# Kernel tuning notes

Hardware: AMD Instinct MI355X
Metric: run time of the kernel (lower is better)

Reference implementation:

```python
import jax, jax.numpy as jnp
import numpy as np

N_NODES = 100000
N_EDGES = 1600000
IN_CH = 128
HEADS = 4
HID = 32
OUT_CH = 128
NEG_SLOPE = 0.2


def setup_inputs() -> dict:
    key = jax.random.key(0)
    ks = jax.random.split(key, 7)
    sc = 1.0 / np.sqrt(IN_CH)
    return {
        "x": jax.random.normal(ks[0], (N_NODES, IN_CH), dtype=jnp.float32),
        "edge_index": jax.random.randint(ks[1], (2, N_EDGES), 0, N_NODES, dtype=jnp.int32),
        "W": jax.random.normal(ks[2], (IN_CH, HEADS * HID), dtype=jnp.float32) * sc,
        "att_src": jax.random.normal(ks[3], (HEADS, HID), dtype=jnp.float32) * sc,
        "att_dst": jax.random.normal(ks[4], (HEADS, HID), dtype=jnp.float32) * sc,
        "lin_w": jax.random.normal(ks[5], (HEADS * HID, OUT_CH), dtype=jnp.float32) * (1.0 / np.sqrt(HEADS * HID)),
        "lin_b": jax.random.normal(ks[6], (OUT_CH,), dtype=jnp.float32) * 0.01,
    }


def reference(x, edge_index, W, att_src, att_dst, lin_w, lin_b):
    N = x.shape[0]
    src, dst = edge_index[0], edge_index[1]
    # node-wise linear transform -> [N, H, C]
    h = (x @ W).reshape(N, HEADS, HID)
    # per-node attention logit components [N, H]
    a_src = jnp.einsum("nhc,hc->nh", h, att_src)
    a_dst = jnp.einsum("nhc,hc->nh", h, att_dst)
    # per-edge logits with LeakyReLU [E, H]
    e = jax.nn.leaky_relu(a_src[src] + a_dst[dst], negative_slope=NEG_SLOPE)
    # segment softmax over destination neighborhoods
    m = jax.ops.segment_max(e, dst, num_segments=N)
    ex = jnp.exp(e - m[dst])
    s = jax.ops.segment_sum(ex, dst, num_segments=N)
    alpha = ex / (s[dst] + 1e-16)
    # weighted scatter-sum of source features [N, H, C] -> concat heads
    msg = h[src] * alpha[:, :, None]
    out = jax.ops.segment_sum(msg, dst, num_segments=N).reshape(N, HEADS * HID)
    # trailing dense + ReLU
    return jax.nn.relu(out @ lin_w + lin_b)
```

## Files before the change

### kernel.cpp

```cpp
#include <hip/hip_runtime.h>
#include <hip/hip_fp16.h>

#define NB   256
#define NBLK 128
#define BSH  9

typedef _Float16 f16;
typedef _Float16 half8 __attribute__((ext_vector_type(8)));
typedef __fp16 pk16x2 __attribute__((ext_vector_type(2)));
typedef float f32x4 __attribute__((ext_vector_type(4)));

__global__ __launch_bounds__(256) void k_setup(
    const float* __restrict__ W, const float* __restrict__ LW,
    f16* __restrict__ Wt, f16* __restrict__ LWt,
    const int* __restrict__ dst, int* __restrict__ bh, int E, int chunk)
{
    int b = blockIdx.x;
    int t = threadIdx.x;
    if (b < 128) {
        if (t < 128) Wt[b * 128 + t]  = (f16)W[t * 128 + b];
        else         LWt[b * 128 + (t - 128)] = (f16)LW[(t - 128) * 128 + b];
        return;
    }
    int blk = b - 128;
    __shared__ int hist[NB];
    hist[t] = 0;
    __syncthreads();
    int e0 = blk * chunk;
    int e1 = min(e0 + chunk, E);
    for (int e = e0 + t; e < e1; e += 256)
        atomicAdd(&hist[dst[e] >> BSH], 1);
    __syncthreads();
    bh[t * NBLK + blk] = hist[t];
}

__global__ __launch_bounds__(256) void k_gemm_att(
    const float* __restrict__ A, const f16* __restrict__ Wt,
    const float* __restrict__ att_s, const float* __restrict__ att_d,
    f16* __restrict__ Hh, float* __restrict__ as_out, float* __restrict__ ad_out,
    int M)
{
    __shared__ __align__(16) f16 as_lds[64 * 136];
    int t = threadIdx.x;
    int row0 = blockIdx.x * 64;

    {
        int r = t >> 2, kq = (t & 3) * 32;
        const float* ap = A + (size_t)(row0 + r) * 128 + kq;
        bool valid = (row0 + r) < M;
        pk16x2 hb[16];
#pragma unroll
        for (int j = 0; j < 8; ++j) {
            float4 v = valid ? *(const float4*)(ap + j * 4) : make_float4(0.f, 0.f, 0.f, 0.f);
            hb[2 * j]     = __builtin_amdgcn_cvt_pkrtz(v.x, v.y);
            hb[2 * j + 1] = __builtin_amdgcn_cvt_pkrtz(v.z, v.w);
        }
        f16* dst = as_lds + r * 136 + kq;
#pragma unroll
        for (int j = 0; j < 4; ++j) *(float4*)(dst + j * 8) = ((float4*)hb)[j];
    }
    __syncthreads();

    int w = t >> 6, ln = t & 63;
    int rr = (w & 1) * 32;
    int cc = (w >> 1) * 64;
    int q = ln >> 4, m = ln & 15;

    f32x4 acc[2][4];
#pragma unroll
    for (int i = 0; i < 2; ++i)
#pragma unroll
        for (int j = 0; j < 4; ++j) acc[i][j] = (f32x4){0.f, 0.f, 0.f, 0.f};

    const f16* wp = Wt + (size_t)(cc + m) * 128 + q * 8;
#pragma unroll
    for (int ks = 0; ks < 4; ++ks) {
        int k0 = ks * 32 + q * 8;
        half8 a0 = *(const half8*)(as_lds + (rr + m) * 136 + k0);
        half8 a1 = *(const half8*)(as_lds + (rr + 16 + m) * 136 + k0);
        half8 bf[4];
#pragma unroll
        for (int j = 0; j < 4; ++j)
            bf[j] = *(const half8*)(wp + j * 16 * 128 + ks * 32);
#pragma unroll
        for (int j = 0; j < 4; ++j) {
            acc[0][j] = __builtin_amdgcn_mfma_f32_16x16x32_f16(a0, bf[j], acc[0][j], 0, 0, 0);
            acc[1][j] = __builtin_amdgcn_mfma_f32_16x16x32_f16(a1, bf[j], acc[1][j], 0, 0, 0);
        }
    }
    __syncthreads();
#pragma unroll
    for (int i = 0; i < 2; ++i)
#pragma unroll
        for (int j = 0; j < 4; ++j)
#pragma unroll
            for (int g = 0; g < 4; ++g)
                as_lds[(rr + i * 16 + q * 4 + g) * 136 + cc + j * 16 + m] = (f16)acc[i][j][g];
    __syncthreads();
    {
        int r = t >> 2, cq = (t & 3) * 32;
        if (row0 + r < M) {
            float4 o0 = *(const float4*)(as_lds + r * 136 + cq);
            float4 o1 = *(const float4*)(as_lds + r * 136 + cq + 8);
            float4 o2 = *(const float4*)(as_lds + r * 136 + cq + 16);
            float4 o3 = *(const float4*)(as_lds + r * 136 + cq + 24);
            float4* hp = (float4*)(Hh + (size_t)(row0 + r) * 128 + cq);
            hp[0] = o0; hp[1] = o1; hp[2] = o2; hp[3] = o3;
        }
    }
    {
        int rl = w * 16 + m;
        int head = q;
        float ds = 0.f, dd = 0.f;
#pragma unroll
        for (int ch = 0; ch < 4; ++ch) {
            half8 hv = *(const half8*)(as_lds + rl * 136 + head * 32 + ch * 8);
            float4 s0 = *(const float4*)(att_s + head * 32 + ch * 8);
            float4 s1 = *(const float4*)(att_s + head * 32 + ch * 8 + 4);
            float4 d0 = *(const float4*)(att_d + head * 32 + ch * 8);
            float4 d1 = *(const float4*)(att_d + head * 32 + ch * 8 + 4);
            ds += (float)hv[0] * s0.x + (float)hv[1] * s0.y + (float)hv[2] * s0.z + (float)hv[3] * s0.w
                + (float)hv[4] * s1.x + (float)hv[5] * s1.y + (float)hv[6] * s1.z + (float)hv[7] * s1.w;
            dd += (float)hv[0] * d0.x + (float)hv[1] * d0.y + (float)hv[2] * d0.z + (float)hv[3] * d0.w
                + (float)hv[4] * d1.x + (float)hv[5] * d1.y + (float)hv[6] * d1.z + (float)hv[7] * d1.w;
        }
        if (row0 + rl < M) {
            as_out[(row0 + rl) * 4 + head] = ds;
            ad_out[(row0 + rl) * 4 + head] = dd;
        }
    }
}


__global__ __launch_bounds__(1024) void k_ph_scan(int* __restrict__ bh)
{
    __shared__ int sd[1024];
    const int per = (NB * NBLK) / 1024;
    int t = threadIdx.x;
    int base = t * per;
    int loc[per];
    int sum = 0;
#pragma unroll
    for (int j = 0; j < per; ++j) { loc[j] = bh[base + j]; sum += loc[j]; }
    sd[t] = sum;
    __syncthreads();
    for (int o = 1; o < 1024; o <<= 1) {
        int x = (t >= o) ? sd[t - o] : 0;
        __syncthreads();
        sd[t] += x;
        __syncthreads();
    }
    int run = sd[t] - sum;
#pragma unroll
    for (int j = 0; j < per; ++j) { bh[base + j] = run; run += loc[j]; }
}

__global__ __launch_bounds__(256) void k_ph_bin(
    const int* __restrict__ ei, const int* __restrict__ bh,
    int* __restrict__ binned, int E, int chunk)
{
    __shared__ int boff[NB];
    int t = threadIdx.x;
    boff[t] = bh[t * NBLK + blockIdx.x];
    __syncthreads();
    int e0 = blockIdx.x * chunk;
    int e1 = min(e0 + chunk, E);
    for (int e = e0 + t; e < e1; e += 256) {
        int s = ei[e];
        int d = ei[E + e];
        int p = atomicAdd(&boff[d >> BSH], 1);
        binned[p] = s | ((d & ((1 << BSH) - 1)) << 17);
    }
}

__global__ __launch_bounds__(256) void k_ph_csr(
    const int* __restrict__ binned, const int* __restrict__ bh,
    int* __restrict__ csr, int* __restrict__ off, int* __restrict__ deg,
    int N, int E)
{
    __shared__ int cnt[512], loff[512], sd[256];
    int b = blockIdx.x;
    int lo = b << BSH;
    if (lo >= N) return;
    int t = threadIdx.x;
    int seg = bh[b * NBLK];
    int segend = (b + 1 < NB) ? bh[(b + 1) * NBLK] : E;
    int len = segend - seg;
    cnt[t] = 0; cnt[t + 256] = 0;
    __syncthreads();
    for (int i = t; i < len; i += 256)
        atomicAdd(&cnt[(unsigned)binned[seg + i] >> 17], 1);
    __syncthreads();
    int a0 = cnt[2 * t], a1 = cnt[2 * t + 1];
    int s = a0 + a1;
    sd[t] = s;
    __syncthreads();
    for (int o = 1; o < 256; o <<= 1) {
        int x = (t >= o) ? sd[t - o] : 0;
        __syncthreads();
        sd[t] += x;
        __syncthreads();
    }
    int ex = sd[t] - s;
    loff[2 * t] = ex;
    loff[2 * t + 1] = ex + a0;
    int n0 = lo + 2 * t;
    if (n0 < N)     { off[n0] = seg + ex;          deg[n0] = a0; }
    if (n0 + 1 < N) { off[n0 + 1] = seg + ex + a0; deg[n0 + 1] = a1; }
    __syncthreads();
    for (int i = t; i < len; i += 256) {
        int v = binned[seg + i];
        int p = atomicAdd(&loff[(unsigned)v >> 17], 1);
        csr[seg + p] = v & 0x1ffff;
    }
}

__global__ __launch_bounds__(256) void k_gather_fused(
    const __half* __restrict__ Hh, const float* __restrict__ as_,
    const float* __restrict__ ad_, const int* __restrict__ off,
    const int* __restrict__ deg, const int* __restrict__ csr,
    const f16* __restrict__ LWt, const float* __restrict__ bias,
    float* __restrict__ Out, int N)
{
    __shared__ __align__(16) __half2 wh[16][68];
    __shared__ int srcs[16][16];
    __shared__ __align__(16) f16 pt[16][136];
    int t = threadIdx.x;
    int wid = t >> 6, lane = t & 63;
    int sub = lane >> 4;
    int li = lane & 15;
    int hh = li >> 2;
    int slot = wid * 4 + sub;
    int gbase = blockIdx.x * 16;
    int n = gbase + slot;
    bool nvalid = n < N;
    int dg = nvalid ? deg[n] : 0;
    int base = nvalid ? off[n] : 0;
    float4 adn = nvalid ? *(const float4*)(ad_ + (size_t)n * 4)
                        : make_float4(0.f, 0.f, 0.f, 0.f);

    float s0 = 0.f, s1 = 0.f, s2 = 0.f, s3 = 0.f;
    float acc[8] = {0.f, 0.f, 0.f, 0.f, 0.f, 0.f, 0.f, 0.f};

    for (int c0 = 0; c0 < dg; c0 += 16) {
        int cnt = min(16, dg - c0);
        {
            int idx = c0 + li;
            int se = csr[base + min(idx, dg - 1)];
            float4 as = *(const float4*)(as_ + (size_t)se * 4);
            float e0 = as.x + adn.x, e1 = as.y + adn.y;
            float e2 = as.z + adn.z, e3 = as.w + adn.w;
            e0 = fmaxf(e0, 0.2f * e0); e1 = fmaxf(e1, 0.2f * e1);
            e2 = fmaxf(e2, 0.2f * e2); e3 = fmaxf(e3, 0.2f * e3);
            float x0 = __expf(e0), x1 = __expf(e1);
            float x2 = __expf(e2), x3 = __expf(e3);
            if (idx >= dg) { x0 = x1 = x2 = x3 = 0.f; }
            s0 += x0; s1 += x1; s2 += x2; s3 += x3;
            __half2 w4[4];
            w4[0] = __float2half2_rn(x0);
            w4[1] = __float2half2_rn(x1);
            w4[2] = __float2half2_rn(x2);
            w4[3] = __float2half2_rn(x3);
            *(float4*)&wh[slot][li * 4] = *(float4*)w4;
            srcs[slot][li] = se;
        }
        __asm__ volatile("s_waitcnt lgkmcnt(0)" ::: "memory");
        int quads = (cnt + 3) >> 2;
        __half2 ah[4];
        ah[0] = ah[1] = ah[2] = ah[3] = __float2half2_rn(0.f);
        for (int qq = 0; qq < quads; ++qq) {
#pragma unroll
            for (int u = 0; u < 4; ++u) {
                int i = qq * 4 + u;
                __half2 w2 = wh[slot][i * 4 + hh];
                int se = srcs[slot][i];
                float4 raw = *(const float4*)(Hh + (size_t)se * 128 + li * 8);
                __half2* ph = (__half2*)&raw;
                ah[0] = __hfma2(ph[0], w2, ah[0]);
                ah[1] = __hfma2(ph[1], w2, ah[1]);
                ah[2] = __hfma2(ph[2], w2, ah[2]);
                ah[3] = __hfma2(ph[3], w2, ah[3]);
            }
            if ((qq & 1) == 1) {
#pragma unroll
                for (int k = 0; k < 4; ++k) {
                    float2 f = __half22float2(ah[k]);
                    acc[2 * k] += f.x; acc[2 * k + 1] += f.y;
                    ah[k] = __float2half2_rn(0.f);
                }
            }
        }
#pragma unroll
        for (int k = 0; k < 4; ++k) {
            float2 f = __half22float2(ah[k]);
            acc[2 * k] += f.x; acc[2 * k + 1] += f.y;
        }
        __asm__ volatile("s_waitcnt lgkmcnt(0)" ::: "memory");
    }

#pragma unroll
    for (int o = 1; o < 16; o <<= 1) {
        s0 += __shfl_xor(s0, o);
        s1 += __shfl_xor(s1, o);
        s2 += __shfl_xor(s2, o);
        s3 += __shfl_xor(s3, o);
    }
    float sh = (hh == 0) ? s0 : (hh == 1) ? s1 : (hh == 2) ? s2 : s3;
    float inv = 1.f / (sh + 1e-16f);
    {
        __half2 o4[4];
#pragma unroll
        for (int k = 0; k < 4; ++k)
            o4[k] = __float22half2_rn(make_float2(acc[2 * k] * inv, acc[2 * k + 1] * inv));
        *(float4*)&pt[slot][li * 8] = *(float4*)o4;
    }
    __syncthreads();

    {
        int cc = wid * 32;
        f32x4 acc2[2];
        acc2[0] = (f32x4){0.f, 0.f, 0.f, 0.f};
        acc2[1] = (f32x4){0.f, 0.f, 0.f, 0.f};
        const f16* wp = LWt + (size_t)(cc + li) * 128 + sub * 8;
#pragma unroll
        for (int ks = 0; ks < 4; ++ks) {
            half8 a0 = *(const half8*)&pt[li][ks * 32 + sub * 8];
            half8 b0 = *(const half8*)(wp + ks * 32);
            half8 b1 = *(const half8*)(wp + 16 * 128 + ks * 32);
            acc2[0] = __builtin_amdgcn_mfma_f32_16x16x32_f16(a0, b0, acc2[0], 0, 0, 0);
            acc2[1] = __builtin_amdgcn_mfma_f32_16x16x32_f16(a0, b1, acc2[1], 0, 0, 0);
        }
        float bv0 = bias[cc + li];
        float bv1 = bias[cc + 16 + li];
#pragma unroll
        for (int g = 0; g < 4; ++g) {
            int r = sub * 4 + g;
            int node = gbase + r;
            if (node < N) {
                Out[(size_t)node * 128 + cc + li]      = fmaxf(acc2[0][g] + bv0, 0.f);
                Out[(size_t)node * 128 + cc + 16 + li] = fmaxf(acc2[1][g] + bv1, 0.f);
            }
        }
    }
}


extern "C" void kernel_launch(void* const* d_in, const int* in_sizes, int n_in,
                              void* d_out, int out_size, void* d_ws, size_t ws_size,
                              hipStream_t stream)
{
    const float* x     = (const float*)d_in[0];
    const int*   ei    = (const int*)d_in[1];
    const float* W     = (const float*)d_in[2];
    const float* att_s = (const float*)d_in[3];
    const float* att_d = (const float*)d_in[4];
    const float* lin_w = (const float*)d_in[5];
    const float* lin_b = (const float*)d_in[6];
    float* out = (float*)d_out;
    int N = in_sizes[0] / 128;
    int E = in_sizes[1] / 2;

    char* p = (char*)d_ws;
    auto alloc = [&](size_t bytes) { char* r = p; p += (bytes + 255) & ~(size_t)255; return r; };
    f16*    Hh   = (f16*)alloc((size_t)N * 128 * 2);
    f16*    Wt   = (f16*)alloc(128 * 128 * 2);
    f16*    LWt  = (f16*)alloc(128 * 128 * 2);
    float*  AS   = (float*)alloc((size_t)N * 4 * 4);
    float*  AD   = (float*)alloc((size_t)N * 4 * 4);
    int*    deg  = (int*)alloc((size_t)N * 4);
    int*    off  = (int*)alloc((size_t)N * 4);
    int*    csr  = (int*)alloc((size_t)E * 4);
    int*    binned = (int*)alloc((size_t)E * 4);
    int*    bh   = (int*)alloc((size_t)NB * NBLK * 4);

    int chunk = (E + NBLK - 1) / NBLK;
    int mb = (N + 63) / 64;
    k_setup<<<256, 256, 0, stream>>>(W, lin_w, Wt, LWt, ei + E, bh, E, chunk);
    k_gemm_att<<<mb, 256, 0, stream>>>(x, Wt, att_s, att_d, Hh, AS, AD, N);
    k_ph_scan<<<1, 1024, 0, stream>>>(bh);
    k_ph_bin<<<NBLK, 256, 0, stream>>>(ei, bh, binned, E, chunk);
    k_ph_csr<<<NB, 256, 0, stream>>>(binned, bh, csr, off, deg, N, E);
    k_gather_fused<<<(N + 15) / 16, 256, 0, stream>>>(
        (const __half*)Hh, AS, AD, off, deg, csr, LWt, lin_b, out, N);
}
```

Baseline: 289.2 us.

## Replace two-level binned CSR build with global-atomic counting sort; fp32 gather accumulation

Drops the LDS-histogram two-pass binning (bin, then per-bin local sort) in favour of a per-node degree count with global atomics, a single-block scan over all N nodes, and an atomic scatter into the CSR. This removes one kernel and the intermediate binned buffer. The cost is heavy global atomic traffic on 1.6M edges, poorer write locality, and a serial per-thread scan of about 100 elements. The gather loop also moves from packed half2 FMA to scalar fp32 FMA with fp32 weights in LDS, which is more accurate but issues more ALU instructions. Neighbour order within each CSR row becomes nondeterministic.

```diff
diff --git a/kernel.cpp b/kernel.cpp
--- a/kernel.cpp
+++ b/kernel.cpp
@@ -1,9 +1,7 @@
 #include <hip/hip_runtime.h>
 #include <hip/hip_fp16.h>
 
-#define NB   256
 #define NBLK 128
-#define BSH  9
 
 typedef _Float16 f16;
 typedef _Float16 half8 __attribute__((ext_vector_type(8)));
@@ -13,25 +11,20 @@
 __global__ __launch_bounds__(256) void k_setup(
     const float* __restrict__ W, const float* __restrict__ LW,
     f16* __restrict__ Wt, f16* __restrict__ LWt,
-    const int* __restrict__ dst, int* __restrict__ bh, int E, int chunk)
+    const int* __restrict__ dst, int* __restrict__ deg, int E, int chunk)
 {
     int b = blockIdx.x;
     int t = threadIdx.x;
     if (b < 128) {
-        if (t < 128) Wt[b * 128 + t]  = (f16)W[t * 128 + b];
-        else         LWt[b * 128 + (t - 128)] = (f16)LW[(t - 128) * 128 + b];
+        if (t < 128) Wt[b * 128 + t]           = (f16)W[t * 128 + b];
+        else         LWt[b * 128 + (t - 128)]  = (f16)LW[(t - 128) * 128 + b];
         return;
     }
     int blk = b - 128;
-    __shared__ int hist[NB];
-    hist[t] = 0;
-    __syncthreads();
     int e0 = blk * chunk;
     int e1 = min(e0 + chunk, E);
     for (int e = e0 + t; e < e1; e += 256)
-        atomicAdd(&hist[dst[e] >> BSH], 1);
-    __syncthreads();
-    bh[t * NBLK + blk] = hist[t];
+        atomicAdd(&deg[dst[e]], 1);
 }
 
 __global__ __launch_bounds__(256) void k_gemm_att(
@@ -131,17 +124,15 @@
     }
 }
 
-
-__global__ __launch_bounds__(1024) void k_ph_scan(int* __restrict__ bh)
+__global__ __launch_bounds__(1024) void k_scan(
+    const int* __restrict__ deg, int* __restrict__ off, int* __restrict__ cur, int N)
 {
     __shared__ int sd[1024];
-    const int per = (NB * NBLK) / 1024;
     int t = threadIdx.x;
-    int base = t * per;
-    int loc[per];
+    int per = (N + 1023) >> 10;
+    int b0 = min(t * per, N), b1 = min(b0 + per, N);
     int sum = 0;
-#pragma unroll
-    for (int j = 0; j < per; ++j) { loc[j] = bh[base + j]; sum += loc[j]; }
+    for (int i = b0; i < b1; ++i) sum += deg[i];
     sd[t] = sum;
     __syncthreads();
     for (int o = 1; o < 1024; o <<= 1) {
@@ -151,67 +142,24 @@
         __syncthreads();
     }
     int run = sd[t] - sum;
-#pragma unroll
-    for (int j = 0; j < per; ++j) { bh[base + j] = run; run += loc[j]; }
-}
-
-__global__ __launch_bounds__(256) void k_ph_bin(
-    const int* __restrict__ ei, const int* __restrict__ bh,
-    int* __restrict__ binned, int E, int chunk)
-{
-    __shared__ int boff[NB];
-    int t = threadIdx.x;
-    boff[t] = bh[t * NBLK + blockIdx.x];
-    __syncthreads();
+    for (int i = b0; i < b1; ++i) {
+        off[i] = run;
+        cur[i] = run;
+        run += deg[i];
+    }
+}
+
+__global__ __launch_bounds__(256) void k_scatter(
+    const int* __restrict__ ei, int* __restrict__ cur,
+    int* __restrict__ csr, int E, int chunk)
+{
     int e0 = blockIdx.x * chunk;
     int e1 = min(e0 + chunk, E);
-    for (int e = e0 + t; e < e1; e += 256) {
+    for (int e = e0 + threadIdx.x; e < e1; e += 256) {
         int s = ei[e];
         int d = ei[E + e];
-        int p = atomicAdd(&boff[d >> BSH], 1);
-        binned[p] = s | ((d & ((1 << BSH) - 1)) << 17);
-    }
-}
-
-__global__ __launch_bounds__(256) void k_ph_csr(
-    const int* __restrict__ binned, const int* __restrict__ bh,
-    int* __restrict__ csr, int* __restrict__ off, int* __restrict__ deg,
-    int N, int E)
-{
-    __shared__ int cnt[512], loff[512], sd[256];
-    int b = blockIdx.x;
-    int lo = b << BSH;
-    if (lo >= N) return;
-    int t = threadIdx.x;
-    int seg = bh[b * NBLK];
-    int segend = (b + 1 < NB) ? bh[(b + 1) * NBLK] : E;
-    int len = segend - seg;
-    cnt[t] = 0; cnt[t + 256] = 0;
-    __syncthreads();
-    for (int i = t; i < len; i += 256)
-        atomicAdd(&cnt[(unsigned)binned[seg + i] >> 17], 1);
-    __syncthreads();
-    int a0 = cnt[2 * t], a1 = cnt[2 * t + 1];
-    int s = a0 + a1;
-    sd[t] = s;
-    __syncthreads();
-    for (int o = 1; o < 256; o <<= 1) {
-        int x = (t >= o) ? sd[t - o] : 0;
-        __syncthreads();
-        sd[t] += x;
-        __syncthreads();
-    }
-    int ex = sd[t] - s;
-    loff[2 * t] = ex;
-    loff[2 * t + 1] = ex + a0;
-    int n0 = lo + 2 * t;
-    if (n0 < N)     { off[n0] = seg + ex;          deg[n0] = a0; }
-    if (n0 + 1 < N) { off[n0 + 1] = seg + ex + a0; deg[n0 + 1] = a1; }
-    __syncthreads();
-    for (int i = t; i < len; i += 256) {
-        int v = binned[seg + i];
-        int p = atomicAdd(&loff[(unsigned)v >> 17], 1);
-        csr[seg + p] = v & 0x1ffff;
+        int p = atomicAdd(&cur[d], 1);
+        csr[p] = s;
     }
 }
 
@@ -222,7 +170,7 @@
     const f16* __restrict__ LWt, const float* __restrict__ bias,
     float* __restrict__ Out, int N)
 {
-    __shared__ __align__(16) __half2 wh[16][68];
+    __shared__ __align__(16) float ws_l[16][68];
     __shared__ int srcs[16][16];
     __shared__ __align__(16) f16 pt[16][136];
     int t = threadIdx.x;
@@ -256,44 +204,29 @@
             float x2 = __expf(e2), x3 = __expf(e3);
             if (idx >= dg) { x0 = x1 = x2 = x3 = 0.f; }
             s0 += x0; s1 += x1; s2 += x2; s3 += x3;
-            __half2 w4[4];
-            w4[0] = __float2half2_rn(x0);
-            w4[1] = __float2half2_rn(x1);
-            w4[2] = __float2half2_rn(x2);
-            w4[3] = __float2half2_rn(x3);
-            *(float4*)&wh[slot][li * 4] = *(float4*)w4;
+            float4 w4 = make_float4(x0, x1, x2, x3);
+            *(float4*)&ws_l[slot][li * 4] = w4;
             srcs[slot][li] = se;
         }
         __asm__ volatile("s_waitcnt lgkmcnt(0)" ::: "memory");
         int quads = (cnt + 3) >> 2;
-        __half2 ah[4];
-        ah[0] = ah[1] = ah[2] = ah[3] = __float2half2_rn(0.f);
         for (int qq = 0; qq < quads; ++qq) {
 #pragma unroll
             for (int u = 0; u < 4; ++u) {
                 int i = qq * 4 + u;
-                __half2 w2 = wh[slot][i * 4 + hh];
+                float w = ws_l[slot][i * 4 + hh];
                 int se = srcs[slot][i];
                 float4 raw = *(const float4*)(Hh + (size_t)se * 128 + li * 8);
                 __half2* ph = (__half2*)&raw;
-                ah[0] = __hfma2(ph[0], w2, ah[0]);
-                ah[1] = __hfma2(ph[1], w2, ah[1]);
-                ah[2] = __hfma2(ph[2], w2, ah[2]);
-                ah[3] = __hfma2(ph[3], w2, ah[3]);
+                acc[0] = fmaf(__low2float(ph[0]),  w, acc[0]);
+                acc[1] = fmaf(__high2float(ph[0]), w, acc[1]);
+                acc[2] = fmaf(__low2float(ph[1]),  w, acc[2]);
+                acc[3] = fmaf(__high2float(ph[1]), w, acc[3]);
+                acc[4] = fmaf(__low2float(ph[2]),  w, acc[4]);
+                acc[5] = fmaf(__high2float(ph[2]), w, acc[5]);
+                acc[6] = fmaf(__low2float(ph[3]),  w, acc[6]);
+                acc[7] = fmaf(__high2float(ph[3]), w, acc[7]);
             }
-            if ((qq & 1) == 1) {
-#pragma unroll
-                for (int k = 0; k < 4; ++k) {
-                    float2 f = __half22float2(ah[k]);
-                    acc[2 * k] += f.x; acc[2 * k + 1] += f.y;
-                    ah[k] = __float2half2_rn(0.f);
-                }
-            }
-        }
-#pragma unroll
-        for (int k = 0; k < 4; ++k) {
-            float2 f = __half22float2(ah[k]);
-            acc[2 * k] += f.x; acc[2 * k + 1] += f.y;
         }
         __asm__ volatile("s_waitcnt lgkmcnt(0)" ::: "memory");
     }
@@ -369,17 +302,16 @@
     float*  AD   = (float*)alloc((size_t)N * 4 * 4);
     int*    deg  = (int*)alloc((size_t)N * 4);
     int*    off  = (int*)alloc((size_t)N * 4);
+    int*    cur  = (int*)alloc((size_t)N * 4);
     int*    csr  = (int*)alloc((size_t)E * 4);
-    int*    binned = (int*)alloc((size_t)E * 4);
-    int*    bh   = (int*)alloc((size_t)NB * NBLK * 4);
 
     int chunk = (E + NBLK - 1) / NBLK;
     int mb = (N + 63) / 64;
-    k_setup<<<256, 256, 0, stream>>>(W, lin_w, Wt, LWt, ei + E, bh, E, chunk);
+    hipMemsetAsync(deg, 0, (size_t)N * 4, stream);
+    k_setup<<<256, 256, 0, stream>>>(W, lin_w, Wt, LWt, ei + E, deg, E, chunk);
     k_gemm_att<<<mb, 256, 0, stream>>>(x, Wt, att_s, att_d, Hh, AS, AD, N);
-    k_ph_scan<<<1, 1024, 0, stream>>>(bh);
-    k_ph_bin<<<NBLK, 256, 0, stream>>>(ei, bh, binned, E, chunk);
-    k_ph_csr<<<NB, 256, 0, stream>>>(binned, bh, csr, off, deg, N, E);
+    k_scan<<<1, 1024, 0, stream>>>(deg, off, cur, N);
+    k_scatter<<<NBLK, 256, 0, stream>>>(ei, cur, csr, E, chunk);
     k_gather_fused<<<(N + 15) / 16, 256, 0, stream>>>(
         (const __half*)Hh, AS, AD, off, deg, csr, LWt, lin_b, out, N);
 }
```

After: 611.9 us. 112% more time.

## Replace per-block histogram scan with global bucket totals and atomic reservation

Applied to the files above, without the earlier changes.

The per-block bucket histogram table and its single-block scan kernel are replaced by global per-bucket totals accumulated with atomics. The binning kernel now rebuilds its own local histogram, scans the totals with wave shuffles, and reserves its slots atomically. This removes one serial launch and lets the histogram and binning passes use more blocks (384 and 512). In exchange, destination indices are read an extra time, a memset is added, and bin order within a bucket becomes nondeterministic.

```diff
diff --git a/kernel.cpp b/kernel.cpp
--- a/kernel.cpp
+++ b/kernel.cpp
@@ -1,9 +1,10 @@
 #include <hip/hip_runtime.h>
 #include <hip/hip_fp16.h>
 
-#define NB   256
-#define NBLK 128
-#define BSH  9
+#define NB    256
+#define BSH   9
+#define HBLK  384
+#define BBLK  512
 
 typedef _Float16 f16;
 typedef _Float16 half8 __attribute__((ext_vector_type(8)));
@@ -13,25 +14,25 @@
 __global__ __launch_bounds__(256) void k_setup(
     const float* __restrict__ W, const float* __restrict__ LW,
     f16* __restrict__ Wt, f16* __restrict__ LWt,
-    const int* __restrict__ dst, int* __restrict__ bh, int E, int chunk)
+    const int* __restrict__ dst, int* __restrict__ btot, int E, int chunk)
 {
     int b = blockIdx.x;
     int t = threadIdx.x;
     if (b < 128) {
-        if (t < 128) Wt[b * 128 + t]  = (f16)W[t * 128 + b];
-        else         LWt[b * 128 + (t - 128)] = (f16)LW[(t - 128) * 128 + b];
+        if (t < 128) Wt[b * 128 + t]           = (f16)W[t * 128 + b];
+        else         LWt[b * 128 + (t - 128)]  = (f16)LW[(t - 128) * 128 + b];
         return;
     }
+    __shared__ int h[NB];
+    h[t] = 0;
+    __syncthreads();
     int blk = b - 128;
-    __shared__ int hist[NB];
-    hist[t] = 0;
-    __syncthreads();
     int e0 = blk * chunk;
     int e1 = min(e0 + chunk, E);
     for (int e = e0 + t; e < e1; e += 256)
-        atomicAdd(&hist[dst[e] >> BSH], 1);
-    __syncthreads();
-    bh[t * NBLK + blk] = hist[t];
+        atomicAdd(&h[dst[e] >> BSH], 1);
+    __syncthreads();
+    if (h[t]) atomicAdd(&btot[t], h[t]);
 }
 
 __global__ __launch_bounds__(256) void k_gemm_att(
@@ -131,63 +132,82 @@
     }
 }
 
-
-__global__ __launch_bounds__(1024) void k_ph_scan(int* __restrict__ bh)
-{
-    __shared__ int sd[1024];
-    const int per = (NB * NBLK) / 1024;
+__global__ __launch_bounds__(256) void k_bin(
+    const int* __restrict__ ei, const int* __restrict__ btot,
+    int* __restrict__ bres, int* __restrict__ binned, int E, int chunk)
+{
+    __shared__ int h[NB];
+    __shared__ int base_s[NB];
+    __shared__ int ws[4];
     int t = threadIdx.x;
-    int base = t * per;
-    int loc[per];
-    int sum = 0;
-#pragma unroll
-    for (int j = 0; j < per; ++j) { loc[j] = bh[base + j]; sum += loc[j]; }
-    sd[t] = sum;
-    __syncthreads();
-    for (int o = 1; o < 1024; o <<= 1) {
-        int x = (t >= o) ? sd[t - o] : 0;
+    {
+        int v = btot[t];
+        int lane = t & 63, w = t >> 6;
+        int x = v;
+#pragma unroll
+        for (int o = 1; o < 64; o <<= 1) {
+            int y = __shfl_up(x, o);
+            if (lane >= o) x += y;
+        }
+        if (lane == 63) ws[w] = x;
         __syncthreads();
-        sd[t] += x;
-        __syncthreads();
-    }
-    int run = sd[t] - sum;
-#pragma unroll
-    for (int j = 0; j < per; ++j) { bh[base + j] = run; run += loc[j]; }
-}
-
-__global__ __launch_bounds__(256) void k_ph_bin(
-    const int* __restrict__ ei, const int* __restrict__ bh,
-    int* __restrict__ binned, int E, int chunk)
-{
-    __shared__ int boff[NB];
-    int t = threadIdx.x;
-    boff[t] = bh[t * NBLK + blockIdx.x];
+        int wb = 0;
+#pragma unroll
+        for (int k = 0; k < 4; ++k) wb += (k < w) ? ws[k] : 0;
+        base_s[t] = wb + x - v;
+    }
+    h[t] = 0;
     __syncthreads();
     int e0 = blockIdx.x * chunk;
     int e1 = min(e0 + chunk, E);
+    for (int e = e0 + t; e < e1; e += 256)
+        atomicAdd(&h[ei[E + e] >> BSH], 1);
+    __syncthreads();
+    int cnt = h[t];
+    int mybase = base_s[t] + (cnt ? atomicAdd(&bres[t], cnt) : 0);
+    __syncthreads();
+    h[t] = mybase;
+    __syncthreads();
     for (int e = e0 + t; e < e1; e += 256) {
         int s = ei[e];
         int d = ei[E + e];
-        int p = atomicAdd(&boff[d >> BSH], 1);
+        int p = atomicAdd(&h[d >> BSH], 1);
         binned[p] = s | ((d & ((1 << BSH) - 1)) << 17);
     }
 }
 
 __global__ __launch_bounds__(256) void k_ph_csr(
-    const int* __restrict__ binned, const int* __restrict__ bh,
+    const int* __restrict__ binned, const int* __restrict__ btot,
     int* __restrict__ csr, int* __restrict__ off, int* __restrict__ deg,
     int N, int E)
 {
     __shared__ int cnt[512], loff[512], sd[256];
+    __shared__ int base_s[NB];
+    __shared__ int ws[4];
     int b = blockIdx.x;
     int lo = b << BSH;
     if (lo >= N) return;
     int t = threadIdx.x;
-    int seg = bh[b * NBLK];
-    int segend = (b + 1 < NB) ? bh[(b + 1) * NBLK] : E;
-    int len = segend - seg;
+    {
+        int v = btot[t];
+        int lane = t & 63, w = t >> 6;
+        int x = v;
+#pragma unroll
+        for (int o = 1; o < 64; o <<= 1) {
+            int y = __shfl_up(x, o);
+            if (lane >= o) x += y;
+        }
+        if (lane == 63) ws[w] = x;
+        __syncthreads();
+        int wb = 0;
+#pragma unroll
+        for (int k = 0; k < 4; ++k) wb += (k < w) ? ws[k] : 0;
+        base_s[t] = wb + x - v;
+    }
     cnt[t] = 0; cnt[t + 256] = 0;
     __syncthreads();
+    int seg = base_s[b];
+    int len = btot[b];
     for (int i = t; i < len; i += 256)
         atomicAdd(&cnt[(unsigned)binned[seg + i] >> 17], 1);
     __syncthreads();
@@ -369,17 +389,19 @@
     float*  AD   = (float*)alloc((size_t)N * 4 * 4);
     int*    deg  = (int*)alloc((size_t)N * 4);
     int*    off  = (int*)alloc((size_t)N * 4);
+    int*    btot = (int*)alloc((size_t)NB * 4 * 2);
+    int*    bres = btot + NB;
     int*    csr  = (int*)alloc((size_t)E * 4);
     int*    binned = (int*)alloc((size_t)E * 4);
-    int*    bh   = (int*)alloc((size_t)NB * NBLK * 4);
-
-    int chunk = (E + NBLK - 1) / NBLK;
+
+    int hchunk = (E + HBLK - 1) / HBLK;
+    int bchunk = (E + BBLK - 1) / BBLK;
     int mb = (N + 63) / 64;
-    k_setup<<<256, 256, 0, stream>>>(W, lin_w, Wt, LWt, ei + E, bh, E, chunk);
+    hipMemsetAsync(btot, 0, (size_t)NB * 4 * 2, stream);
+    k_setup<<<128 + HBLK, 256, 0, stream>>>(W, lin_w, Wt, LWt, ei + E, btot, E, hchunk);
     k_gemm_att<<<mb, 256, 0, stream>>>(x, Wt, att_s, att_d, Hh, AS, AD, N);
-    k_ph_scan<<<1, 1024, 0, stream>>>(bh);
-    k_ph_bin<<<NBLK, 256, 0, stream>>>(ei, bh, binned, E, chunk);
-    k_ph_csr<<<NB, 256, 0, stream>>>(binned, bh, csr, off, deg, N, E);
+    k_bin<<<BBLK, 256, 0, stream>>>(ei, btot, bres, binned, E, bchunk);
+    k_ph_csr<<<NB, 256, 0, stream>>>(binned, btot, csr, off, deg, N, E);
     k_gather_fused<<<(N + 15) / 16, 256, 0, stream>>>(
         (const __half*)Hh, AS, AD, off, deg, csr, LWt, lin_b, out, N);
 }
```

Measured after the change: 280.5 us. 1.03x faster.
